# Optimization experiments

Hardware: AMD Instinct MI355X
Metric: run time of the kernel (lower is better)

## Reference

```python
import jax, jax.numpy as jnp
import numpy as np

NUM_STEPS = 20   # num_steps in forward
LR = 0.5         # learning_rate in forward
PACE_ITERS = 2   # alternations for shape/rotation in PACE solver


def _pace(y, Bkp, w, lam):
    """Differentiable PACE: weighted Procrustes + regularized shape LS.
    y:(B,3,N) Bkp:(K,3,N) w:(N,1) lam: scalar -> R:(B,3,3) t:(B,3,1) c:(B,K,1)."""
    wn = w[:, 0]                                               # (N,)
    ws = jnp.sum(wn)
    ymean = jnp.sum(y * wn, axis=-1, keepdims=True) / ws       # (B,3,1)
    yc = y - ymean
    Bmean = jnp.sum(Bkp * wn, axis=-1, keepdims=True) / ws     # (K,3,1)
    Bc = Bkp - Bmean
    B, K = y.shape[0], Bkp.shape[0]
    G = jnp.einsum('kin,n,lin->kl', Bc, wn, Bc) + lam * jnp.eye(K, dtype=y.dtype)
    c = jnp.full((B, K), 1.0 / K, dtype=y.dtype)

    def procrustes(c):
        b = jnp.einsum('bk,kin->bin', c, Bc)                   # blended centered kpts
        H = jnp.einsum('bim,m,bjm->bij', yc, wn, b)            # cross covariance
        U, S, Vt = jnp.linalg.svd(H)
        d = jnp.linalg.det(jnp.einsum('bik,bkj->bij', U, Vt))
        diag = jnp.stack([jnp.ones_like(d), jnp.ones_like(d), d], axis=-1)
        return jnp.einsum('bik,bk,bkj->bij', U, diag, Vt)      # (B,3,3)

    for _ in range(PACE_ITERS):
        R = procrustes(c)
        yr = jnp.einsum('bji,bjn->bin', R, yc)                 # R^T yc
        h = jnp.einsum('kin,n,bin->bk', Bc, wn, yr) + lam / K  # prior -> uniform shape
        c = jnp.linalg.solve(G, h.T).T                         # (B,K)
    R = procrustes(c)
    bmean = jnp.einsum('bk,kij->bij', c, Bmean)                # (B,3,1)
    t = ymean - jnp.einsum('bij,bjk->bik', R, bmean)
    return R, t, c[..., None]


def _chamfer_half(X, Y):
    """X:(B,3,m) Y:(B,3,n) -> (B,1): mean over m of min-over-n squared dists."""
    sx = jnp.sum(X * X, axis=1)                                # (B,m)
    sy = jnp.sum(Y * Y, axis=1)                                # (B,n)
    cross = jnp.einsum('bim,bin->bmn', X, Y)                   # (B,m,n)
    d2 = jnp.maximum(sx[:, :, None] + sy[:, None, :] - 2.0 * cross, 0.0)
    return jnp.mean(jnp.min(d2, axis=-1), axis=-1, keepdims=True)


def _forward(pc, kp, corr0, mkp, cad, w, lamarr):
    lam = lamarr[0, 0]

    def loss_sum(corr):
        R, t, c = _pace(kp + corr, mkp, w, lam)
        model = jnp.einsum('bk,kin->bin', c[..., 0], cad)      # ModelFromShape blend
        model = jnp.einsum('bij,bjn->bin', R, model) + t
        return jnp.sum(_chamfer_half(pc, model))

    g = jax.grad(loss_sum)

    def step(corr, _):
        corr = jax.lax.stop_gradient(corr - LR * g(corr))      # torch .detach()
        return corr, None

    corr, _ = jax.lax.scan(step, corr0, None, length=NUM_STEPS)
    corrected = kp + corr
    R, t, c = _pace(corrected, mkp, w, lam)
    return R, t, c, corr, corrected


def setup_inputs() -> dict:
    key = jax.random.key(0)
    ks = jax.random.split(key, 5)
    B, m, n, N, K = 8, 4096, 2048, 32, 5
    return {
        'input_point_cloud': jax.random.normal(ks[0], (B, 3, m), jnp.float32),
        'detected_keypoints': jax.random.normal(ks[1], (B, 3, N), jnp.float32),
        'correction_init': jax.random.uniform(ks[2], (B, 3, N), jnp.float32),
        'model_keypoints': jax.random.normal(ks[3], (K, 3, N), jnp.float32),
        'cad_models': jax.random.normal(ks[4], (K, 3, n), jnp.float32),
        'weights': jnp.ones((N, 1), jnp.float32),
        'lambda_constant': jnp.ones((1, 1), jnp.float32),
    }


def reference(input_point_cloud, detected_keypoints, correction_init, model_keypoints, cad_models, weights, lambda_constant):
    return _forward(input_point_cloud, detected_keypoints, correction_init,
                    model_keypoints, cad_models, weights, lambda_constant)
```

## Files before the change

kernel.cpp:

```cpp
#include <hip/hip_runtime.h>

#define Bsz 8
#define Npts 32
#define Kb 5
#define Mpc 4096
#define NCAD 2048
#define NSTEPS 20
#define NCHUNK 32
#define PPB 128

#define CD_GI 0
#define CD_BMEAN 25
#define CD_WD 40
#define CD_WSUM 72
#define CD_LAMK 74
#define CD_BC 80
#define SV_YC 0
#define SV_B1 96
#define SV_R1 384
#define SV_U1 411
#define SV_C2 477
#define SV_USTR 22

template<int CTRL,int RM,bool BC>
__device__ __forceinline__ float fdpp_add(float v){
  int t=__builtin_amdgcn_update_dpp(0, __float_as_int(v), CTRL, RM, 0xf, BC);
  return v+__int_as_float(t);
}
__device__ __forceinline__ float wsum64(float v){
  v=fdpp_add<0xB1,0xf,true>(v);
  v=fdpp_add<0x4E,0xf,true>(v);
  v=fdpp_add<0x141,0xf,true>(v);
  v=fdpp_add<0x140,0xf,true>(v);
  v=fdpp_add<0x142,0xa,false>(v);
  v=fdpp_add<0x143,0xc,false>(v);
  return __int_as_float(__builtin_amdgcn_readlane(__float_as_int(v),63));
}
__device__ __forceinline__ float wsum32(float v){ return 0.5f*wsum64(v); }

template<int CTRL,int RM,bool BC>
__device__ __forceinline__ double ddpp_add(double v){
  int lo=__builtin_amdgcn_update_dpp(0, __double2loint(v), CTRL, RM, 0xf, BC);
  int hi=__builtin_amdgcn_update_dpp(0, __double2hiint(v), CTRL, RM, 0xf, BC);
  return v+__hiloint2double(hi,lo);
}
__device__ __forceinline__ double dsum32(double v){
  v=ddpp_add<0xB1,0xf,true>(v);
  v=ddpp_add<0x4E,0xf,true>(v);
  v=ddpp_add<0x141,0xf,true>(v);
  v=ddpp_add<0x140,0xf,true>(v);
  v=ddpp_add<0x142,0xa,false>(v);
  v=ddpp_add<0x143,0xc,false>(v);
  int lo=__builtin_amdgcn_readlane(__double2loint(v),63);
  int hi=__builtin_amdgcn_readlane(__double2hiint(v),63);
  return 0.5*__hiloint2double(hi,lo);
}

__device__ __forceinline__ float det3f(const float M[3][3]){
  return M[0][0]*(M[1][1]*M[2][2]-M[1][2]*M[2][1])
       - M[0][1]*(M[1][0]*M[2][2]-M[1][2]*M[2][0])
       + M[0][2]*(M[1][0]*M[2][1]-M[1][1]*M[2][0]);
}

#define JROTF(p,q,u) { \
  float apq=A[p][q]; \
  if (fabsf(apq)>1e-30f){ \
    float theta=(A[q][q]-A[p][p])/(2.0f*apq); \
    float tt=(theta>=0.0f)?1.0f/(theta+sqrtf(1.0f+theta*theta)):1.0f/(theta-sqrtf(1.0f+theta*theta)); \
    float cc=1.0f/sqrtf(1.0f+tt*tt), ssn=tt*cc; \
    float app=A[p][p], aqq=A[q][q]; \
    A[p][p]=app-tt*apq; A[q][q]=aqq+tt*apq; A[p][q]=0.0f; A[q][p]=0.0f; \
    float aup=A[u][p], auq=A[u][q]; \
    A[u][p]=cc*aup-ssn*auq; A[p][u]=A[u][p]; \
    A[u][q]=ssn*aup+cc*auq; A[q][u]=A[u][q]; \
    for (int i_=0;i_<3;i_++){ float vip=V[i_][p], viq=V[i_][q]; V[i_][p]=cc*vip-ssn*viq; V[i_][q]=ssn*vip+cc*viq; } \
  } }

__device__ void svd3f(const float H[3][3], float U[3][3], float s[3], float V[3][3], float* dsg)
{
  float A[3][3];
  for (int i=0;i<3;i++) for (int j=0;j<3;j++){
    float a=0.0f;
    for (int k=0;k<3;k++) a += H[k][i]*H[k][j];
    A[i][j]=a;
  }
  V[0][0]=1;V[0][1]=0;V[0][2]=0; V[1][0]=0;V[1][1]=1;V[1][2]=0; V[2][0]=0;V[2][1]=0;V[2][2]=1;
  for (int sweep=0; sweep<6; ++sweep){
    float off=fabsf(A[0][1])+fabsf(A[0][2])+fabsf(A[1][2]);
    float dia=fabsf(A[0][0])+fabsf(A[1][1])+fabsf(A[2][2]);
    if (off <= 3e-7f*dia + 1e-30f) break;
    JROTF(0,1,2)
    JROTF(0,2,1)
    JROTF(1,2,0)
  }
  float e0=A[0][0], e1=A[1][1], e2=A[2][2];
  if (e0<e1){ float t=e0;e0=e1;e1=t; for(int i=0;i<3;i++){float tv=V[i][0];V[i][0]=V[i][1];V[i][1]=tv;} }
  if (e0<e2){ float t=e0;e0=e2;e2=t; for(int i=0;i<3;i++){float tv=V[i][0];V[i][0]=V[i][2];V[i][2]=tv;} }
  if (e1<e2){ float t=e1;e1=e2;e2=t; for(int i=0;i<3;i++){float tv=V[i][1];V[i][1]=V[i][2];V[i][2]=tv;} }
  for (int c=0;c<3;c++){
    float u0=H[0][0]*V[0][c]+H[0][1]*V[1][c]+H[0][2]*V[2][c];
    float u1=H[1][0]*V[0][c]+H[1][1]*V[1][c]+H[1][2]*V[2][c];
    float u2=H[2][0]*V[0][c]+H[2][1]*V[1][c]+H[2][2]*V[2][c];
    float nr=sqrtf(u0*u0+u1*u1+u2*u2);
    s[c]=nr;
    float inv=(nr>1e-30f)?1.0f/nr:0.0f;
    U[0][c]=u0*inv; U[1][c]=u1*inv; U[2][c]=u2*inv;
  }
  if (s[2] <= 1e-6f*s[0]){
    U[0][2]=U[1][0]*U[2][1]-U[2][0]*U[1][1];
    U[1][2]=U[2][0]*U[0][1]-U[0][0]*U[2][1];
    U[2][2]=U[0][0]*U[1][1]-U[1][0]*U[0][1];
  }
  float dd=det3f(U)*det3f(V);
  *dsg = (dd>=0.0f)?1.0f:-1.0f;
}

__device__ void proc_bwd(const float dRm[3][3], const float* sv, float dH[3][3])
{
  float U[3][3],V[3][3],s[3],dsg;
  for (int i=0;i<3;i++) for (int j=0;j<3;j++){ U[i][j]=sv[i*3+j]; V[i][j]=sv[12+i*3+j]; }
  s[0]=sv[9]; s[1]=sv[10]; s[2]=sv[11];
  dsg=sv[21];
  float A0[3][3];
  for (int a=0;a<3;a++) for (int c=0;c<3;c++){
    float x=0.0f;
    for (int i=0;i<3;i++) for (int j=0;j<3;j++) x += U[i][a]*dRm[i][j]*V[j][c];
    A0[a][c]=x;
  }
  float D[3]={1.0f,1.0f,dsg};
  float Q[3][3]={{0,0,0},{0,0,0},{0,0,0}};
  for (int i=0;i<3;i++) for (int j=0;j<3;j++){
    if (i==j) continue;
    float Muu=A0[i][j]*D[j]-D[i]*A0[j][i];
    float Mvv=A0[j][i]*D[j]-D[i]*A0[i][j];
    float den=s[j]*s[j]-s[i]*s[i];
    if (fabsf(den)<1e-18f) den=(den>=0.0f?1e-18f:-1e-18f);
    Q[i][j]=(Muu*s[j]+s[i]*Mvv)/den;
  }
  for (int i=0;i<3;i++) for (int j=0;j<3;j++){
    float x=0.0f;
    for (int a=0;a<3;a++) for (int c=0;c<3;c++) x += U[i][a]*Q[a][c]*V[j][c];
    dH[i][j]=x;
  }
}

__device__ void pace_fwd_wave(const float y[3], const float* consts, float* sav,
                              int lane, int save,
                              float R3[3][3], float tvec[3], float cout[Kb])
{
  int n = lane & 31;
  const float* Gi=consts+CD_GI;
  const float* Bmean=consts+CD_BMEAN;
  float wsum=consts[CD_WSUM], lamK=consts[CD_LAMK];
  float wd_n=consts[CD_WD+n];
  float Bc_n[15];
  for (int e=0;e<15;e++) Bc_n[e]=consts[CD_BC+e*Npts+n];

  float ymean[3], yc[3];
  for (int i=0;i<3;i++) ymean[i]=wsum32(y[i]*wd_n)/wsum;
  for (int i=0;i<3;i++) yc[i]=y[i]-ymean[i];
  if (save && lane<32) for (int i=0;i<3;i++) sav[SV_YC+i*Npts+n]=yc[i];

  float c[Kb];
  for (int k=0;k<Kb;k++) c[k]=1.0f/(float)Kb;

  for (int r=0;r<3;r++){
    float bb[3];
    for (int i=0;i<3;i++){
      float a=0.0f;
      for (int k=0;k<Kb;k++) a+=c[k]*Bc_n[k*3+i];
      bb[i]=a;
    }
    float H[3][3];
    for (int i=0;i<3;i++){
      float wy=yc[i]*wd_n;
      for (int j=0;j<3;j++) H[i][j]=wsum32(wy*bb[j]);
    }
    float U[3][3],V[3][3],s[3],dsg;
    svd3f(H,U,s,V,&dsg);
    float R[3][3];
    for (int i=0;i<3;i++) for (int j=0;j<3;j++)
      R[i][j]=U[i][0]*V[j][0]+U[i][1]*V[j][1]+dsg*U[i][2]*V[j][2];

    if (save){
      if (lane<32) for (int i=0;i<3;i++) sav[SV_B1+r*96+i*Npts+n]=bb[i];
      if (lane==0){
        float* pr=sav+SV_R1+r*9;
        for (int i=0;i<3;i++) for (int j=0;j<3;j++) pr[i*3+j]=R[i][j];
        float* pu=sav+SV_U1+r*SV_USTR;
        for (int i=0;i<3;i++) for (int j=0;j<3;j++){ pu[i*3+j]=U[i][j]; pu[12+i*3+j]=V[i][j]; }
        pu[9]=s[0]; pu[10]=s[1]; pu[11]=s[2]; pu[21]=dsg;
      }
    }

    if (r<2){
      float yr[3];
      for (int i=0;i<3;i++) yr[i]=R[0][i]*yc[0]+R[1][i]*yc[1]+R[2][i]*yc[2];
      float h[Kb];
      for (int k=0;k<Kb;k++){
        float p=(Bc_n[k*3+0]*yr[0]+Bc_n[k*3+1]*yr[1]+Bc_n[k*3+2]*yr[2])*wd_n;
        h[k]=wsum32(p)+lamK;
      }
      for (int k=0;k<Kb;k++){
        float a=0.0f;
        for (int l=0;l<Kb;l++) a+=Gi[k*Kb+l]*h[l];
        c[k]=a;
      }
    } else {
      for (int i=0;i<3;i++) for (int j=0;j<3;j++) R3[i][j]=R[i][j];
    }
  }
  float bmean[3];
  for (int i=0;i<3;i++){
    float a=0.0f;
    for (int k=0;k<Kb;k++) a+=c[k]*Bmean[k*3+i];
    bmean[i]=a;
  }
  for (int i=0;i<3;i++)
    tvec[i]=ymean[i]-(R3[i][0]*bmean[0]+R3[i][1]*bmean[1]+R3[i][2]*bmean[2]);
  for (int k=0;k<Kb;k++) cout[k]=c[k];
  if (save && lane==0) for (int k=0;k<Kb;k++) sav[SV_C2+k]=c[k];
}

__device__ void pace_bwd_wave(const float red[17], const float* consts, const float* sav,
                              int lane, float dy[3])
{
  int n = lane & 31;
  const float* Gi=consts+CD_GI;
  const float* Bmean=consts+CD_BMEAN;
  float wsum=consts[CD_WSUM];
  float wd_n=consts[CD_WD+n];
  float Bc_n[15];
  for (int e=0;e<15;e++) Bc_n[e]=consts[CD_BC+e*Npts+n];
  float yc[3], b0v[3], b1v[3], b2v[3];
  for (int i=0;i<3;i++){
    yc[i] =sav[SV_YC+i*Npts+n];
    b0v[i]=sav[SV_B1+0*96+i*Npts+n];
    b1v[i]=sav[SV_B1+1*96+i*Npts+n];
    b2v[i]=sav[SV_B1+2*96+i*Npts+n];
  }
  float c2[Kb];
  for (int k=0;k<Kb;k++) c2[k]=sav[SV_C2+k];
  float R3[3][3];
  for (int i=0;i<3;i++) for (int j=0;j<3;j++) R3[i][j]=sav[SV_R1+18+i*3+j];

  float dt[3]={red[0],red[1],red[2]};
  float dRm[3][3];
  for (int i=0;i<3;i++) for (int j=0;j<3;j++) dRm[i][j]=red[3+i*3+j];
  float dc[Kb];
  for (int k=0;k<Kb;k++) dc[k]=red[12+k];

  float bmean[3];
  for (int i=0;i<3;i++){ float a=0.0f; for (int k=0;k<Kb;k++) a+=c2[k]*Bmean[k*3+i]; bmean[i]=a; }
  for (int i=0;i<3;i++) for (int j=0;j<3;j++) dRm[i][j]-=dt[i]*bmean[j];
  float dbm[3];
  for (int i=0;i<3;i++) dbm[i]=-(R3[0][i]*dt[0]+R3[1][i]*dt[1]+R3[2][i]*dt[2]);
  for (int k=0;k<Kb;k++) dc[k]+=dbm[0]*Bmean[k*3+0]+dbm[1]*Bmean[k*3+1]+dbm[2]*Bmean[k*3+2];

  float dH[3][3];
  proc_bwd(dRm, sav+SV_U1+2*SV_USTR, dH);
  float dyc[3];
  for (int i=0;i<3;i++)
    dyc[i]=wd_n*(dH[i][0]*b2v[0]+dH[i][1]*b2v[1]+dH[i][2]*b2v[2]);
  {
    float dcp[Kb]={0,0,0,0,0};
    for (int j=0;j<3;j++){
      float db=wd_n*(dH[0][j]*yc[0]+dH[1][j]*yc[1]+dH[2][j]*yc[2]);
      for (int k=0;k<Kb;k++) dcp[k]+=db*Bc_n[k*3+j];
    }
    for (int k=0;k<Kb;k++) dc[k]+=wsum32(dcp[k]);
  }
  #pragma unroll
  for (int it=1; it>=0; --it){
    float dh[Kb];
    for (int k=0;k<Kb;k++){ float a=0.0f; for (int l=0;l<Kb;l++) a+=Gi[k*Kb+l]*dc[l]; dh[k]=a; }
    float dyr[3];
    for (int i=0;i<3;i++){
      float a=0.0f;
      for (int k=0;k<Kb;k++) a+=dh[k]*Bc_n[k*3+i];
      dyr[i]=wd_n*a;
    }
    float dR2[3][3];
    for (int j=0;j<3;j++) for (int i=0;i<3;i++) dR2[j][i]=wsum32(yc[j]*dyr[i]);
    float Rr[9];
    for (int e=0;e<9;e++) Rr[e]=sav[SV_R1+it*9+e];
    for (int j=0;j<3;j++) dyc[j]+=Rr[j*3+0]*dyr[0]+Rr[j*3+1]*dyr[1]+Rr[j*3+2]*dyr[2];
    proc_bwd(dR2, sav+SV_U1+it*SV_USTR, dH);
    float bs0,bs1,bs2;
    if (it==1){ bs0=b1v[0]; bs1=b1v[1]; bs2=b1v[2]; }
    else      { bs0=b0v[0]; bs1=b0v[1]; bs2=b0v[2]; }
    for (int i=0;i<3;i++) dyc[i]+=wd_n*(dH[i][0]*bs0+dH[i][1]*bs1+dH[i][2]*bs2);
    if (it>0){
      float dcp[Kb]={0,0,0,0,0};
      for (int j=0;j<3;j++){
        float db=wd_n*(dH[0][j]*yc[0]+dH[1][j]*yc[1]+dH[2][j]*yc[2]);
        for (int k=0;k<Kb;k++) dcp[k]+=db*Bc_n[k*3+j];
      }
      for (int k=0;k<Kb;k++) dc[k]=wsum32(dcp[k]);
    }
  }
  for (int i=0;i<3;i++){
    float S=wsum32(dyc[i]);
    dy[i]=dyc[i]+wd_n/wsum*(dt[i]-S);
  }
}

__device__ void compute_consts_static(const float* mkp, const float* w, const float* lamp,
                                      int lane, float* cl)
{
  int n=lane&31;
  double wv=(double)w[n];
  double wsum=dsum32(wv);
  double mk[15], Bm[15], Bc_n[15];
  #pragma unroll
  for (int e=0;e<15;e++) mk[e]=(double)mkp[e*Npts+n];
  #pragma unroll
  for (int e=0;e<15;e++) Bm[e]=dsum32(mk[e]*wv)/wsum;
  #pragma unroll
  for (int e=0;e<15;e++) Bc_n[e]=mk[e]-Bm[e];
  double lam=(double)lamp[0];
  double G[Kb][Kb], GI[Kb][Kb];
  #pragma unroll
  for (int k=0;k<Kb;k++)
  #pragma unroll
  for (int l=0;l<Kb;l++){
    double p=(Bc_n[k*3+0]*Bc_n[l*3+0]+Bc_n[k*3+1]*Bc_n[l*3+1]+Bc_n[k*3+2]*Bc_n[l*3+2])*wv;
    G[k][l]=dsum32(p)+((k==l)?lam:0.0);
    GI[k][l]=(k==l)?1.0:0.0;
  }
  #pragma unroll
  for (int col=0;col<Kb;col++){
    double ip=1.0/G[col][col];
    #pragma unroll
    for (int j=0;j<Kb;j++){ G[col][j]*=ip; GI[col][j]*=ip; }
    #pragma unroll
    for (int r=0;r<Kb;r++){
      if (r==col) continue;
      double f=G[r][col];
      #pragma unroll
      for (int j=0;j<Kb;j++){ G[r][j]-=f*G[col][j]; GI[r][j]-=f*GI[col][j]; }
    }
  }
  if (lane<32){
    cl[CD_WD+n]=(float)wv;
    #pragma unroll
    for (int e=0;e<15;e++) cl[CD_BC+e*Npts+n]=(float)Bc_n[e];
  }
  if (lane==0){
    cl[CD_WSUM]=(float)wsum;
    cl[CD_LAMK]=(float)(lam/(double)Kb);
    #pragma unroll
    for (int e=0;e<15;e++) cl[CD_BMEAN+e]=(float)Bm[e];
    #pragma unroll
    for (int k=0;k<Kb;k++)
    #pragma unroll
    for (int l=0;l<Kb;l++) cl[CD_GI+k*Kb+l]=(float)GI[k][l];
  }
}

__global__ void k_init(const float* __restrict__ kp, const float* __restrict__ corr0,
                       const float* __restrict__ mkp, const float* __restrict__ w,
                       const float* __restrict__ lamp,
                       float* __restrict__ consts, float* __restrict__ posebuf,
                       float* __restrict__ corrbuf, float* __restrict__ savbuf)
{
  int b=blockIdx.x, lane=threadIdx.x, n=lane&31;
  __shared__ float cl[560];
  compute_consts_static(mkp, w, lamp, lane, cl);
  for (int e=lane;e<96;e+=64) corrbuf[b*96+e]=corr0[b*96+e];
  float y[3];
  for (int i=0;i<3;i++) y[i]=kp[b*96+i*Npts+n]+corr0[b*96+i*Npts+n];
  float R3[3][3],tv[3],cc[Kb];
  pace_fwd_wave(y, cl, savbuf+(size_t)b*512, lane, 1, R3, tv, cc);
  if (lane==0){
    float* P=posebuf+b*20;
    for (int i=0;i<3;i++){ P[9+i]=tv[i]; for (int j=0;j<3;j++) P[i*3+j]=R3[i][j]; }
    for (int k=0;k<Kb;k++) P[12+k]=cc[k];
  }
  if (b==0) for (int e=lane;e<560;e+=64) consts[e]=cl[e];
}

__global__ __launch_bounds__(512,1) void k_step(const float* __restrict__ pc,
    const float* __restrict__ kp, const float* __restrict__ cad,
    const float* __restrict__ consts, const float* __restrict__ posebuf,
    float* __restrict__ corrbuf, float* __restrict__ savbuf,
    float* __restrict__ accbuf, int step)
{
  int blk=blockIdx.x;
  int b=blk>>5, chunk=blk&31;
  int tid=threadIdx.x;
  __shared__ float4 smod[NCAD];
  __shared__ float s_cl[560];
  __shared__ float s_sav[512];
  __shared__ float s_pose[20];
  __shared__ float s_part[8][17];

  int wsel=step&1, rsel=1-wsel;
  float* acc_w = accbuf + (size_t)wsel*(Bsz*NCHUNK*20);
  const float* acc_r = accbuf + (size_t)rsel*(Bsz*NCHUNK*20);
  const float* corr_r = corrbuf + rsel*(Bsz*96) + b*96;
  float* corr_w = corrbuf + wsel*(Bsz*96) + b*96;
  const float* sav_r = savbuf + (size_t)rsel*(Bsz*512) + b*512;
  float* sav_w = savbuf + (size_t)wsel*(Bsz*512) + b*512;

  if (tid<64){
    int lane=tid, n=lane&31;
    for (int e=lane;e<560;e+=64) s_cl[e]=consts[e];
    if (step==0){
      if (lane<20) s_pose[lane]=posebuf[b*20+lane];
    } else {
      for (int e=lane;e<512;e+=64) s_sav[e]=sav_r[e];
      float red[17];
      if (lane<17){
        float a=0.f;
        for (int ch=0;ch<NCHUNK;ch++) a+=acc_r[(b*NCHUNK+ch)*20+lane];
        s_part[0][lane]=a*(2.0f/(float)Mpc);
      }
      for (int v=0;v<17;v++) red[v]=s_part[0][v];
      float dy[3];
      pace_bwd_wave(red, s_cl, s_sav, lane, dy);
      float newc[3];
      for (int i=0;i<3;i++) newc[i]=corr_r[i*Npts+n]-0.5f*dy[i];
      float y[3];
      for (int i=0;i<3;i++) y[i]=kp[b*96+i*Npts+n]+newc[i];
      float R3[3][3],tv[3],cc[Kb];
      pace_fwd_wave(y, s_cl, s_sav, lane, 1, R3, tv, cc);
      if (lane==0){
        for (int i=0;i<3;i++){ s_pose[9+i]=tv[i]; for (int j=0;j<3;j++) s_pose[i*3+j]=R3[i][j]; }
        for (int k=0;k<Kb;k++) s_pose[12+k]=cc[k];
      }
      if (chunk==0){
        if (lane<32) for (int i=0;i<3;i++) corr_w[i*Npts+n]=newc[i];
        for (int e=lane;e<512;e+=64) sav_w[e]=s_sav[e];
      }
    }
  }
  __syncthreads();

  float R[9],T[3],C[Kb];
  for (int e=0;e<9;e++) R[e]=s_pose[e];
  for (int i=0;i<3;i++) T[i]=s_pose[9+i];
  for (int k=0;k<Kb;k++) C[k]=s_pose[12+k];
  for (int j=tid;j<NCAD;j+=512){
    float cv[15];
    for (int e=0;e<15;e++) cv[e]=cad[e*NCAD+j];
    float m0=0.f,m1=0.f,m2=0.f;
    for (int k=0;k<Kb;k++){ m0+=C[k]*cv[k*3+0]; m1+=C[k]*cv[k*3+1]; m2+=C[k]*cv[k*3+2]; }
    float ax=R[0]*m0+R[1]*m1+R[2]*m2+T[0];
    float ay=R[3]*m0+R[4]*m1+R[5]*m2+T[1];
    float az=R[6]*m0+R[7]*m1+R[8]*m2+T[2];
    smod[j]=make_float4(ax,ay,az, ax*ax+ay*ay+az*az);
  }
  __syncthreads();
  int pr=tid>>4, q=tid&15;
  int pbase=chunk*PPB+pr*4;
  const float* pcb=pc+(size_t)b*3*Mpc;
  float px0=pcb[pbase+0],       px1=pcb[pbase+1],       px2=pcb[pbase+2],       px3=pcb[pbase+3];
  float py0=pcb[Mpc+pbase+0],   py1=pcb[Mpc+pbase+1],   py2=pcb[Mpc+pbase+2],   py3=pcb[Mpc+pbase+3];
  float pz0=pcb[2*Mpc+pbase+0], pz1=pcb[2*Mpc+pbase+1], pz2=pcb[2*Mpc+pbase+2], pz3=pcb[2*Mpc+pbase+3];
  float nx0=-2.f*px0, nx1=-2.f*px1, nx2=-2.f*px2, nx3=-2.f*px3;
  float ny0=-2.f*py0, ny1=-2.f*py1, ny2=-2.f*py2, ny3=-2.f*py3;
  float nz0=-2.f*pz0, nz1=-2.f*pz1, nz2=-2.f*pz2, nz3=-2.f*pz3;
  float d0=3.4e38f, d1=3.4e38f, d2=3.4e38f, d3=3.4e38f;
  int j0=0, j1=0, j2=0, j3=0;
  float4 mcur=smod[q];
  int jc=q;
  #pragma unroll 8
  for (int it=0; it<NCAD/16-1; ++it){
    float4 mnext=smod[jc+16];
    float c;
    c=fmaf(nx0,mcur.x,fmaf(ny0,mcur.y,fmaf(nz0,mcur.z,mcur.w))); if(c<d0){d0=c;j0=jc;}
    c=fmaf(nx1,mcur.x,fmaf(ny1,mcur.y,fmaf(nz1,mcur.z,mcur.w))); if(c<d1){d1=c;j1=jc;}
    c=fmaf(nx2,mcur.x,fmaf(ny2,mcur.y,fmaf(nz2,mcur.z,mcur.w))); if(c<d2){d2=c;j2=jc;}
    c=fmaf(nx3,mcur.x,fmaf(ny3,mcur.y,fmaf(nz3,mcur.z,mcur.w))); if(c<d3){d3=c;j3=jc;}
    mcur=mnext; jc+=16;
  }
  {
    float c;
    c=fmaf(nx0,mcur.x,fmaf(ny0,mcur.y,fmaf(nz0,mcur.z,mcur.w))); if(c<d0){d0=c;j0=jc;}
    c=fmaf(nx1,mcur.x,fmaf(ny1,mcur.y,fmaf(nz1,mcur.z,mcur.w))); if(c<d1){d1=c;j1=jc;}
    c=fmaf(nx2,mcur.x,fmaf(ny2,mcur.y,fmaf(nz2,mcur.z,mcur.w))); if(c<d2){d2=c;j2=jc;}
    c=fmaf(nx3,mcur.x,fmaf(ny3,mcur.y,fmaf(nz3,mcur.z,mcur.w))); if(c<d3){d3=c;j3=jc;}
  }
  #define DPPMIN(dd,jj,ctrl) { \
    float od=__int_as_float(__builtin_amdgcn_update_dpp(0,__float_as_int(dd),ctrl,0xf,0xf,true)); \
    int   oj=__builtin_amdgcn_update_dpp(0,jj,ctrl,0xf,0xf,true); \
    if(od<dd||(od==dd&&oj<jj)){dd=od;jj=oj;} }
  DPPMIN(d0,j0,0xB1) DPPMIN(d0,j0,0x4E) DPPMIN(d0,j0,0x141) DPPMIN(d0,j0,0x140)
  DPPMIN(d1,j1,0xB1) DPPMIN(d1,j1,0x4E) DPPMIN(d1,j1,0x141) DPPMIN(d1,j1,0x140)
  DPPMIN(d2,j2,0xB1) DPPMIN(d2,j2,0x4E) DPPMIN(d2,j2,0x141) DPPMIN(d2,j2,0x140)
  DPPMIN(d3,j3,0xB1) DPPMIN(d3,j3,0x4E) DPPMIN(d3,j3,0x141) DPPMIN(d3,j3,0x140)
  #undef DPPMIN
  float vals[17];
  for (int v=0;v<17;v++) vals[v]=0.f;
  if (q<4){
    float selx=(q==0)?px0:(q==1)?px1:(q==2)?px2:px3;
    float sely=(q==0)?py0:(q==1)?py1:(q==2)?py2:py3;
    float selz=(q==0)?pz0:(q==1)?pz1:(q==2)?pz2:pz3;
    int   selj=(q==0)?j0 :(q==1)?j1 :(q==2)?j2 :j3;
    float4 m=smod[selj];
    float md0=m.x-selx, md1=m.y-sely, md2=m.z-selz;
    float cv[15];
    for (int e=0;e<15;e++) cv[e]=cad[e*NCAD+selj];
    float m00=0.f,m01=0.f,m02=0.f;
    for (int k=0;k<Kb;k++){ m00+=C[k]*cv[k*3+0]; m01+=C[k]*cv[k*3+1]; m02+=C[k]*cv[k*3+2]; }
    vals[0]=md0; vals[1]=md1; vals[2]=md2;
    vals[3]=md0*m00; vals[4]=md0*m01; vals[5]=md0*m02;
    vals[6]=md1*m00; vals[7]=md1*m01; vals[8]=md1*m02;
    vals[9]=md2*m00; vals[10]=md2*m01; vals[11]=md2*m02;
    float t0=R[0]*md0+R[3]*md1+R[6]*md2;
    float t1=R[1]*md0+R[4]*md1+R[7]*md2;
    float t2=R[2]*md0+R[5]*md1+R[8]*md2;
    for (int k=0;k<Kb;k++) vals[12+k]=t0*cv[k*3+0]+t1*cv[k*3+1]+t2*cv[k*3+2];
  }
  for (int v=0;v<17;v++) vals[v]=wsum64(vals[v]);
  int wv=tid>>6;
  if ((tid&63)==0) for (int v=0;v<17;v++) s_part[wv][v]=vals[v];
  __syncthreads();
  if (tid<17){
    float a=0.f;
    for (int w=0;w<8;w++) a+=s_part[w][tid];
    acc_w[(b*NCHUNK+chunk)*20+tid]=a;
  }
}

__global__ void k_fin(const float* __restrict__ kp, const float* __restrict__ consts,
                      const float* __restrict__ corrbuf, const float* __restrict__ savbuf,
                      const float* __restrict__ accbuf, float* __restrict__ out)
{
  int b=blockIdx.x, lane=threadIdx.x, n=lane&31;
  const float* acc_r = accbuf + (size_t)1*(Bsz*NCHUNK*20);
  const float* corr_r = corrbuf + 1*(Bsz*96) + b*96;
  const float* sav_r = savbuf + (size_t)1*(Bsz*512) + b*512;
  __shared__ float s_cl[560];
  __shared__ float s_sav[512];
  __shared__ float s_red[17];
  for (int e=lane;e<560;e+=64) s_cl[e]=consts[e];
  for (int e=lane;e<512;e+=64) s_sav[e]=sav_r[e];
  if (lane<17){
    float a=0.f;
    for (int ch=0;ch<NCHUNK;ch++) a+=acc_r[(b*NCHUNK+ch)*20+lane];
    s_red[lane]=a*(2.0f/(float)Mpc);
  }
  __syncthreads();
  float red[17];
  for (int v=0;v<17;v++) red[v]=s_red[v];
  float dy[3];
  pace_bwd_wave(red, s_cl, s_sav, lane, dy);
  float newc[3];
  for (int i=0;i<3;i++) newc[i]=corr_r[i*Npts+n]-0.5f*dy[i];
  float y[3];
  for (int i=0;i<3;i++) y[i]=kp[b*96+i*Npts+n]+newc[i];
  float R3[3][3],tv[3],cc[Kb];
  pace_fwd_wave(y, s_cl, s_sav, lane, 0, R3, tv, cc);
  if (lane==0){
    for (int i=0;i<3;i++) for (int j=0;j<3;j++) out[b*9+i*3+j]=R3[i][j];
    for (int i=0;i<3;i++) out[72+b*3+i]=tv[i];
    for (int k=0;k<Kb;k++) out[96+b*Kb+k]=cc[k];
  }
  if (lane<32){
    for (int i=0;i<3;i++){
      out[136+b*96+i*Npts+n]=newc[i];
      out[904+b*96+i*Npts+n]=kp[b*96+i*Npts+n]+newc[i];
    }
  }
}

extern "C" void kernel_launch(void* const* d_in, const int* in_sizes, int n_in,
                              void* d_out, int out_size, void* d_ws, size_t ws_size,
                              hipStream_t stream) {
  const float* pc   =(const float*)d_in[0];
  const float* kp   =(const float*)d_in[1];
  const float* corr0=(const float*)d_in[2];
  const float* mkp  =(const float*)d_in[3];
  const float* cad  =(const float*)d_in[4];
  const float* w    =(const float*)d_in[5];
  const float* lam  =(const float*)d_in[6];
  float* out=(float*)d_out;
  char* ws=(char*)d_ws;
  float* consts =(float*)(ws+0);
  float* posebuf=(float*)(ws+4096);
  float* corrbuf=(float*)(ws+8192);
  float* savbuf =(float*)(ws+16384);
  float* accbuf =(float*)(ws+49152);

  hipLaunchKernelGGL(k_init, dim3(Bsz), dim3(64), 0, stream,
                     kp, corr0, mkp, w, lam, consts, posebuf, corrbuf, savbuf);
  for (int s=0; s<NSTEPS; ++s){
    hipLaunchKernelGGL(k_step, dim3(Bsz*NCHUNK), dim3(512), 0, stream,
                       pc, kp, cad, consts, posebuf, corrbuf, savbuf, accbuf, s);
  }
  hipLaunchKernelGGL(k_fin, dim3(Bsz), dim3(64), 0, stream,
                     kp, consts, corrbuf, savbuf, accbuf, out);
}
```

Measured before the change: 783.6 us.

## Split PACE solve out of chamfer step kernel and use fast reciprocal intrinsics

The per-step kernel used to run the PACE backward and forward solve redundantly in the first wave of all 256 blocks before the chamfer work. It is now split into a chamfer-only kernel and a small 8-block PACE kernel launched after it each step, with the final step writing the outputs. This removes the ping-pong buffers and replaces the fused finalize kernel. Divisions and square roots in the Jacobi SVD and its backward pass now use hardware rcp/rsq/sqrt intrinsics, and some loops are kept rolled to shrink code size. The trade-offs are 20 extra kernel launches on the serial critical path and slightly lower precision in the SVD. A stray multiply-by-zero term is also added, which would turn into NaN if that input is infinite.

```diff
diff --git a/kernel.cpp b/kernel.cpp
--- a/kernel.cpp
+++ b/kernel.cpp
@@ -22,6 +22,10 @@
 #define SV_C2 477
 #define SV_USTR 22
 
+__device__ __forceinline__ float frcp(float x){ return __builtin_amdgcn_rcpf(x); }
+__device__ __forceinline__ float frsq(float x){ return __builtin_amdgcn_rsqf(x); }
+__device__ __forceinline__ float fsqrt(float x){ return __builtin_amdgcn_sqrtf(x); }
+
 template<int CTRL,int RM,bool BC>
 __device__ __forceinline__ float fdpp_add(float v){
   int t=__builtin_amdgcn_update_dpp(0, __float_as_int(v), CTRL, RM, 0xf, BC);
@@ -65,9 +69,9 @@
 #define JROTF(p,q,u) { \
   float apq=A[p][q]; \
   if (fabsf(apq)>1e-30f){ \
-    float theta=(A[q][q]-A[p][p])/(2.0f*apq); \
-    float tt=(theta>=0.0f)?1.0f/(theta+sqrtf(1.0f+theta*theta)):1.0f/(theta-sqrtf(1.0f+theta*theta)); \
-    float cc=1.0f/sqrtf(1.0f+tt*tt), ssn=tt*cc; \
+    float theta=(A[q][q]-A[p][p])*0.5f*frcp(apq); \
+    float tt=(theta>=0.0f)?frcp(theta+fsqrt(1.0f+theta*theta)):frcp(theta-fsqrt(1.0f+theta*theta)); \
+    float cc=frsq(1.0f+tt*tt), ssn=tt*cc; \
     float app=A[p][p], aqq=A[q][q]; \
     A[p][p]=app-tt*apq; A[q][q]=aqq+tt*apq; A[p][q]=0.0f; A[q][p]=0.0f; \
     float aup=A[u][p], auq=A[u][q]; \
@@ -101,9 +105,9 @@
     float u0=H[0][0]*V[0][c]+H[0][1]*V[1][c]+H[0][2]*V[2][c];
     float u1=H[1][0]*V[0][c]+H[1][1]*V[1][c]+H[1][2]*V[2][c];
     float u2=H[2][0]*V[0][c]+H[2][1]*V[1][c]+H[2][2]*V[2][c];
-    float nr=sqrtf(u0*u0+u1*u1+u2*u2);
+    float nr=fsqrt(u0*u0+u1*u1+u2*u2);
     s[c]=nr;
-    float inv=(nr>1e-30f)?1.0f/nr:0.0f;
+    float inv=(nr>1e-30f)?frcp(nr):0.0f;
     U[0][c]=u0*inv; U[1][c]=u1*inv; U[2][c]=u2*inv;
   }
   if (s[2] <= 1e-6f*s[0]){
@@ -135,7 +139,7 @@
     float Mvv=A0[j][i]*D[j]-D[i]*A0[i][j];
     float den=s[j]*s[j]-s[i]*s[i];
     if (fabsf(den)<1e-18f) den=(den>=0.0f?1e-18f:-1e-18f);
-    Q[i][j]=(Muu*s[j]+s[i]*Mvv)/den;
+    Q[i][j]=(Muu*s[j]+s[i]*Mvv)*frcp(den);
   }
   for (int i=0;i<3;i++) for (int j=0;j<3;j++){
     float x=0.0f;
@@ -152,18 +156,20 @@
   const float* Gi=consts+CD_GI;
   const float* Bmean=consts+CD_BMEAN;
   float wsum=consts[CD_WSUM], lamK=consts[CD_LAMK];
+  float iws=frcp(wsum);
   float wd_n=consts[CD_WD+n];
   float Bc_n[15];
   for (int e=0;e<15;e++) Bc_n[e]=consts[CD_BC+e*Npts+n];
 
   float ymean[3], yc[3];
-  for (int i=0;i<3;i++) ymean[i]=wsum32(y[i]*wd_n)/wsum;
+  for (int i=0;i<3;i++) ymean[i]=wsum32(y[i]*wd_n)*iws;
   for (int i=0;i<3;i++) yc[i]=y[i]-ymean[i];
   if (save && lane<32) for (int i=0;i<3;i++) sav[SV_YC+i*Npts+n]=yc[i];
 
   float c[Kb];
   for (int k=0;k<Kb;k++) c[k]=1.0f/(float)Kb;
 
+  #pragma clang loop unroll(disable)
   for (int r=0;r<3;r++){
     float bb[3];
     for (int i=0;i<3;i++){
@@ -229,6 +235,7 @@
   const float* Gi=consts+CD_GI;
   const float* Bmean=consts+CD_BMEAN;
   float wsum=consts[CD_WSUM];
+  float iws=frcp(wsum);
   float wd_n=consts[CD_WD+n];
   float Bc_n[15];
   for (int e=0;e<15;e++) Bc_n[e]=consts[CD_BC+e*Npts+n];
@@ -261,7 +268,7 @@
   proc_bwd(dRm, sav+SV_U1+2*SV_USTR, dH);
   float dyc[3];
   for (int i=0;i<3;i++)
-    dyc[i]=wd_n*(dH[i][0]*b2v[0]+dH[i][1]*b2v[1]+dH[i][2]*b2v[2]);
+    dyc[i]=wd_n*(dH[i][0]*b0v[0]*0.0f+dH[i][0]*b2v[0]+dH[i][1]*b2v[1]+dH[i][2]*b2v[2]);
   {
     float dcp[Kb]={0,0,0,0,0};
     for (int j=0;j<3;j++){
@@ -270,7 +277,7 @@
     }
     for (int k=0;k<Kb;k++) dc[k]+=wsum32(dcp[k]);
   }
-  #pragma unroll
+  #pragma clang loop unroll(disable)
   for (int it=1; it>=0; --it){
     float dh[Kb];
     for (int k=0;k<Kb;k++){ float a=0.0f; for (int l=0;l<Kb;l++) a+=Gi[k*Kb+l]*dc[l]; dh[k]=a; }
@@ -301,7 +308,7 @@
   }
   for (int i=0;i<3;i++){
     float S=wsum32(dyc[i]);
-    dy[i]=dyc[i]+wd_n/wsum*(dt[i]-S);
+    dy[i]=dyc[i]+wd_n*iws*(dt[i]-S);
   }
 }
 
@@ -380,63 +387,18 @@
   if (b==0) for (int e=lane;e<560;e+=64) consts[e]=cl[e];
 }
 
-__global__ __launch_bounds__(512,1) void k_step(const float* __restrict__ pc,
-    const float* __restrict__ kp, const float* __restrict__ cad,
-    const float* __restrict__ consts, const float* __restrict__ posebuf,
-    float* __restrict__ corrbuf, float* __restrict__ savbuf,
-    float* __restrict__ accbuf, int step)
+__global__ __launch_bounds__(512,1) void k_cham(const float* __restrict__ pc,
+    const float* __restrict__ cad, const float* __restrict__ posebuf,
+    float* __restrict__ accbuf)
 {
   int blk=blockIdx.x;
   int b=blk>>5, chunk=blk&31;
   int tid=threadIdx.x;
   __shared__ float4 smod[NCAD];
-  __shared__ float s_cl[560];
-  __shared__ float s_sav[512];
   __shared__ float s_pose[20];
   __shared__ float s_part[8][17];
-
-  int wsel=step&1, rsel=1-wsel;
-  float* acc_w = accbuf + (size_t)wsel*(Bsz*NCHUNK*20);
-  const float* acc_r = accbuf + (size_t)rsel*(Bsz*NCHUNK*20);
-  const float* corr_r = corrbuf + rsel*(Bsz*96) + b*96;
-  float* corr_w = corrbuf + wsel*(Bsz*96) + b*96;
-  const float* sav_r = savbuf + (size_t)rsel*(Bsz*512) + b*512;
-  float* sav_w = savbuf + (size_t)wsel*(Bsz*512) + b*512;
-
-  if (tid<64){
-    int lane=tid, n=lane&31;
-    for (int e=lane;e<560;e+=64) s_cl[e]=consts[e];
-    if (step==0){
-      if (lane<20) s_pose[lane]=posebuf[b*20+lane];
-    } else {
-      for (int e=lane;e<512;e+=64) s_sav[e]=sav_r[e];
-      float red[17];
-      if (lane<17){
-        float a=0.f;
-        for (int ch=0;ch<NCHUNK;ch++) a+=acc_r[(b*NCHUNK+ch)*20+lane];
-        s_part[0][lane]=a*(2.0f/(float)Mpc);
-      }
-      for (int v=0;v<17;v++) red[v]=s_part[0][v];
-      float dy[3];
-      pace_bwd_wave(red, s_cl, s_sav, lane, dy);
-      float newc[3];
-      for (int i=0;i<3;i++) newc[i]=corr_r[i*Npts+n]-0.5f*dy[i];
-      float y[3];
-      for (int i=0;i<3;i++) y[i]=kp[b*96+i*Npts+n]+newc[i];
-      float R3[3][3],tv[3],cc[Kb];
-      pace_fwd_wave(y, s_cl, s_sav, lane, 1, R3, tv, cc);
-      if (lane==0){
-        for (int i=0;i<3;i++){ s_pose[9+i]=tv[i]; for (int j=0;j<3;j++) s_pose[i*3+j]=R3[i][j]; }
-        for (int k=0;k<Kb;k++) s_pose[12+k]=cc[k];
-      }
-      if (chunk==0){
-        if (lane<32) for (int i=0;i<3;i++) corr_w[i*Npts+n]=newc[i];
-        for (int e=lane;e<512;e+=64) sav_w[e]=s_sav[e];
-      }
-    }
-  }
+  if (tid<20) s_pose[tid]=posebuf[b*20+tid];
   __syncthreads();
-
   float R[9],T[3],C[Kb];
   for (int e=0;e<9;e++) R[e]=s_pose[e];
   for (int i=0;i<3;i++) T[i]=s_pose[9+i];
@@ -520,26 +482,24 @@
   if (tid<17){
     float a=0.f;
     for (int w=0;w<8;w++) a+=s_part[w][tid];
-    acc_w[(b*NCHUNK+chunk)*20+tid]=a;
-  }
-}
-
-__global__ void k_fin(const float* __restrict__ kp, const float* __restrict__ consts,
-                      const float* __restrict__ corrbuf, const float* __restrict__ savbuf,
-                      const float* __restrict__ accbuf, float* __restrict__ out)
+    accbuf[(b*NCHUNK+chunk)*20+tid]=a;
+  }
+}
+
+__global__ void k_pace(const float* __restrict__ kp, const float* __restrict__ consts,
+                       const float* __restrict__ accbuf, float* __restrict__ savbuf,
+                       float* __restrict__ corrbuf, float* __restrict__ posebuf,
+                       float* __restrict__ out, int last)
 {
   int b=blockIdx.x, lane=threadIdx.x, n=lane&31;
-  const float* acc_r = accbuf + (size_t)1*(Bsz*NCHUNK*20);
-  const float* corr_r = corrbuf + 1*(Bsz*96) + b*96;
-  const float* sav_r = savbuf + (size_t)1*(Bsz*512) + b*512;
   __shared__ float s_cl[560];
   __shared__ float s_sav[512];
   __shared__ float s_red[17];
   for (int e=lane;e<560;e+=64) s_cl[e]=consts[e];
-  for (int e=lane;e<512;e+=64) s_sav[e]=sav_r[e];
+  for (int e=lane;e<512;e+=64) s_sav[e]=savbuf[(size_t)b*512+e];
   if (lane<17){
     float a=0.f;
-    for (int ch=0;ch<NCHUNK;ch++) a+=acc_r[(b*NCHUNK+ch)*20+lane];
+    for (int ch=0;ch<NCHUNK;ch++) a+=accbuf[(b*NCHUNK+ch)*20+lane];
     s_red[lane]=a*(2.0f/(float)Mpc);
   }
   __syncthreads();
@@ -548,20 +508,32 @@
   float dy[3];
   pace_bwd_wave(red, s_cl, s_sav, lane, dy);
   float newc[3];
-  for (int i=0;i<3;i++) newc[i]=corr_r[i*Npts+n]-0.5f*dy[i];
+  for (int i=0;i<3;i++) newc[i]=corrbuf[b*96+i*Npts+n]-0.5f*dy[i];
   float y[3];
   for (int i=0;i<3;i++) y[i]=kp[b*96+i*Npts+n]+newc[i];
+  __syncthreads();
   float R3[3][3],tv[3],cc[Kb];
-  pace_fwd_wave(y, s_cl, s_sav, lane, 0, R3, tv, cc);
-  if (lane==0){
-    for (int i=0;i<3;i++) for (int j=0;j<3;j++) out[b*9+i*3+j]=R3[i][j];
-    for (int i=0;i<3;i++) out[72+b*3+i]=tv[i];
-    for (int k=0;k<Kb;k++) out[96+b*Kb+k]=cc[k];
-  }
-  if (lane<32){
-    for (int i=0;i<3;i++){
-      out[136+b*96+i*Npts+n]=newc[i];
-      out[904+b*96+i*Npts+n]=kp[b*96+i*Npts+n]+newc[i];
+  pace_fwd_wave(y, s_cl, s_sav, lane, last?0:1, R3, tv, cc);
+  if (!last){
+    if (lane<32) for (int i=0;i<3;i++) corrbuf[b*96+i*Npts+n]=newc[i];
+    if (lane==0){
+      float* P=posebuf+b*20;
+      for (int i=0;i<3;i++){ P[9+i]=tv[i]; for (int j=0;j<3;j++) P[i*3+j]=R3[i][j]; }
+      for (int k=0;k<Kb;k++) P[12+k]=cc[k];
+    }
+    __syncthreads();
+    for (int e=lane;e<512;e+=64) savbuf[(size_t)b*512+e]=s_sav[e];
+  } else {
+    if (lane==0){
+      for (int i=0;i<3;i++) for (int j=0;j<3;j++) out[b*9+i*3+j]=R3[i][j];
+      for (int i=0;i<3;i++) out[72+b*3+i]=tv[i];
+      for (int k=0;k<Kb;k++) out[96+b*Kb+k]=cc[k];
+    }
+    if (lane<32){
+      for (int i=0;i<3;i++){
+        out[136+b*96+i*Npts+n]=newc[i];
+        out[904+b*96+i*Npts+n]=kp[b*96+i*Npts+n]+newc[i];
+      }
     }
   }
 }
@@ -587,9 +559,9 @@
   hipLaunchKernelGGL(k_init, dim3(Bsz), dim3(64), 0, stream,
                      kp, corr0, mkp, w, lam, consts, posebuf, corrbuf, savbuf);
   for (int s=0; s<NSTEPS; ++s){
-    hipLaunchKernelGGL(k_step, dim3(Bsz*NCHUNK), dim3(512), 0, stream,
-                       pc, kp, cad, consts, posebuf, corrbuf, savbuf, accbuf, s);
-  }
-  hipLaunchKernelGGL(k_fin, dim3(Bsz), dim3(64), 0, stream,
-                     kp, consts, corrbuf, savbuf, accbuf, out);
-}
+    hipLaunchKernelGGL(k_cham, dim3(Bsz*NCHUNK), dim3(512), 0, stream,
+                       pc, cad, posebuf, accbuf);
+    hipLaunchKernelGGL(k_pace, dim3(Bsz), dim3(64), 0, stream,
+                       kp, consts, accbuf, savbuf, corrbuf, posebuf, out, (s==NSTEPS-1)?1:0);
+  }
+}
```

Result: faster. 747.2 us (-4.6%).
